# Kernel tuning notes

Measured on AMD Instinct MI355X. Metric: run time of the kernel, lower is better.

The kernel has to match this reference:

```python
import jax, jax.numpy as jnp
import numpy as np

T, B, IN_DIM = 8192, 4, 512
D_V, D_K, CHUNK = 512, 64, 128
EPS = 1e-8


def setup_inputs() -> dict:
    key = jax.random.key(0)
    ks = jax.random.split(key, 9)
    s = 0.02
    return {
        "x": jax.random.normal(ks[0], (T, B, IN_DIM), jnp.float32),
        "Wv": jax.random.normal(ks[1], (D_V, IN_DIM), jnp.float32) * s,
        "bv": jnp.zeros((D_V,), jnp.float32),
        "Wk": jax.random.normal(ks[2], (D_K, IN_DIM), jnp.float32) * s,
        "bk": jnp.zeros((D_K,), jnp.float32),
        "Wq": jax.random.normal(ks[3], (D_K, IN_DIM), jnp.float32) * s,
        "bq": jnp.zeros((D_K,), jnp.float32),
        "Wa": jax.random.normal(ks[4], (D_K, IN_DIM), jnp.float32) * s,
        "ba": jnp.zeros((D_K,), jnp.float32),
    }


def reference(x, Wv, bv, Wk, bk, Wq, bq, Wa, ba):
    # Projections: x (T, B, in_dim)
    v = x @ Wv.T + bv                      # (T, B, d)
    k = x @ Wk.T + bk                      # (T, B, n)
    q = x @ Wq.T + bq                      # (T, B, n)
    alpha = jax.nn.sigmoid(x @ Wa.T + ba)  # (T, B, n) decay gates

    Tt, Bb = x.shape[0], x.shape[1]
    C = CHUNK
    nC = Tt // C  # T assumed divisible by chunk size

    def to_chunks(a):
        return a.reshape(nC, C, Bb, a.shape[-1])

    vs, ks_, qs, als = to_chunks(v), to_chunks(k), to_chunks(q), to_chunks(alpha)
    causal = jnp.tril(jnp.ones((C, C), dtype=bool))  # (C, C)

    def body(S, inp):
        v_ch, k_ch, q_ch, a_ch = inp  # each (C, B, .)
        # Cumulative decay product within chunk (clamped as in the original)
        p = jnp.cumprod(jnp.maximum(a_ch, EPS), axis=0)      # (C, B, n)
        q_t = q_ch * p                                        # (C, B, n)
        k_t = k_ch / (p + EPS)                                # (C, B, n)
        # Intra-chunk causal attention scores
        A = jnp.einsum('tbn,sbn->bts', q_t, k_t)              # (B, C, C)
        A = jnp.where(causal[None, :, :], A, jnp.zeros((), A.dtype))
        y = jnp.einsum('bts,sbd->tbd', A, v_ch)               # intra-chunk
        y = y + jnp.einsum('bdn,tbn->tbd', S, q_t)            # cross-chunk carry
        # State update to end of chunk
        p_end = p[-1]                                         # (B, n)
        S_writes = jnp.einsum('tbd,tbn->bdn', v_ch, k_t * p_end[None, :, :])
        S_new = S * p_end[:, None, :] + S_writes              # (B, d, n)
        return S_new, y

    S0 = jnp.zeros((Bb, D_V, D_K), x.dtype)
    _, ys = jax.lax.scan(body, S0, (vs, ks_, qs, als))        # ys: (nC, C, B, d)
    return ys.reshape(Tt, Bb, D_V)
```

## Files before the change

### kernel.cpp

```cpp
#include <hip/hip_runtime.h>
#include <math.h>

#define T_DIM 8192
#define B_DIM 4
#define INDIM 512
#define DV 512
#define DK 64
#define CHUNK 128
#define NCH (T_DIM / CHUNK)
#define ROWS (T_DIM * B_DIM)
#define NPAD 768
#define KCAT 192
#define EPSF 1e-8f

typedef float float4_t __attribute__((ext_vector_type(4)));
typedef short short8_t __attribute__((ext_vector_type(8)));
typedef _Float16 half8_t __attribute__((ext_vector_type(8)));

__device__ inline unsigned short f2bf(float f) {
  unsigned int u = __float_as_uint(f);
  unsigned int r = (u + 0x7fffu + ((u >> 16) & 1u)) >> 16;
  return (unsigned short)r;
}
__device__ inline float bf2f(unsigned short h) {
  return __uint_as_float(((unsigned int)h) << 16);
}
__device__ inline unsigned short f2h(float f) {
  _Float16 h = (_Float16)f;
  unsigned short u;
  __builtin_memcpy(&u, &h, 2);
  return u;
}

__device__ inline void gload16(const void* g, void* l) {
  __builtin_amdgcn_global_load_lds(
      (const __attribute__((address_space(1))) void*)g,
      (__attribute__((address_space(3))) void*)l, 16, 0, 0);
}

__global__ __launch_bounds__(256) void cast_kernel(
    const float* __restrict__ x,
    const float* __restrict__ Wv, const float* __restrict__ Wk,
    const float* __restrict__ Wq, const float* __restrict__ Wa,
    const float* __restrict__ bv, const float* __restrict__ bk,
    const float* __restrict__ bq, const float* __restrict__ ba,
    unsigned short* __restrict__ xh, unsigned short* __restrict__ wh,
    float* __restrict__ bcat)
{
  if (blockIdx.x < 16384) {
    const size_t i4 = ((size_t)blockIdx.x * 256 + threadIdx.x) * 4;
    const float4 v = *(const float4*)&x[i4];
    ushort4 h;
    h.x = f2h(v.x); h.y = f2h(v.y); h.z = f2h(v.z); h.w = f2h(v.w);
    *(ushort4*)&xh[i4] = h;
  } else {
    const int t = (blockIdx.x - 16384) * 256 + threadIdx.x;
    const size_t i4 = (size_t)t * 4;
    const int row = (int)(i4 >> 9);
    const int col = (int)(i4 & 511);
    float4 v = {0.f, 0.f, 0.f, 0.f};
    if (row < 512)      v = *(const float4*)&Wv[(size_t)row * INDIM + col];
    else if (row < 576) v = *(const float4*)&Wk[(size_t)(row - 512) * INDIM + col];
    else if (row < 640) v = *(const float4*)&Wq[(size_t)(row - 576) * INDIM + col];
    else if (row < 704) v = *(const float4*)&Wa[(size_t)(row - 640) * INDIM + col];
    ushort4 h;
    h.x = f2h(v.x); h.y = f2h(v.y); h.z = f2h(v.z); h.w = f2h(v.w);
    *(ushort4*)&wh[i4] = h;
    if (t < NPAD) {
      float b = 0.f;
      if (t < 512)      b = bv[t];
      else if (t < 576) b = bk[t - 512];
      else if (t < 640) b = bq[t - 576];
      else if (t < 704) b = ba[t - 640];
      bcat[t] = b;
    }
  }
}

__global__ __launch_bounds__(256) void proj_mfma_kernel(
    const unsigned short* __restrict__ xh, const unsigned short* __restrict__ wh,
    const float* __restrict__ bcat,
    float* __restrict__ v_ws, float* __restrict__ k_ws,
    float* __restrict__ q_ws, float* __restrict__ a_ws)
{
  __shared__ __align__(16) _Float16 Ah[3][128 * 32];
  __shared__ __align__(16) _Float16 Bh[3][128 * 32];

  const int d     = blockIdx.x;
  const int grp   = d >> 3;
  const int ytile = (d & 7) * 32 + grp / 6;
  const int xtile = grp % 6;
  const int r0 = ytile * 128;
  const int c0 = xtile * 128;

  const int tid  = threadIdx.x;
  const int wave = tid >> 6, lane = tid & 63;
  const int wm   = (wave & 1) * 64, wn = (wave >> 1) * 64;
  const int fm   = lane & 15;
  const int fk   = (lane >> 4) * 8;

  float4_t acc[4][4];
#pragma unroll
  for (int i = 0; i < 4; ++i)
#pragma unroll
    for (int j = 0; j < 4; ++j) acc[i][j] = (float4_t)0.0f;

  const int srow = tid >> 2;
  const int scol = (tid & 3) * 8;

  const unsigned short* pA0 = xh + (size_t)(r0 + srow) * INDIM + scol;
  const unsigned short* pA1 = xh + (size_t)(r0 + 64 + srow) * INDIM + scol;
  const unsigned short* pB0 = wh + (size_t)(c0 + srow) * INDIM + scol;
  const unsigned short* pB1 = wh + (size_t)(c0 + 64 + srow) * INDIM + scol;

  auto stage = [&](int buf, int k0) {
    gload16(pA0 + k0, &Ah[buf][tid * 8]);
    gload16(pA1 + k0, &Ah[buf][(256 + tid) * 8]);
    gload16(pB0 + k0, &Bh[buf][tid * 8]);
    gload16(pB1 + k0, &Bh[buf][(256 + tid) * 8]);
  };

  auto compute = [&](int buf) {
    half8_t a[4], b[4];
#pragma unroll
    for (int i = 0; i < 4; ++i)
      a[i] = *(const half8_t*)&Ah[buf][(wm + i * 16 + fm) * 32 + fk];
#pragma unroll
    for (int j = 0; j < 4; ++j)
      b[j] = *(const half8_t*)&Bh[buf][(wn + j * 16 + fm) * 32 + fk];
    __builtin_amdgcn_s_setprio(1);
#pragma unroll
    for (int i = 0; i < 4; ++i)
#pragma unroll
      for (int j = 0; j < 4; ++j)
        acc[i][j] = __builtin_amdgcn_mfma_f32_16x16x32_f16(a[i], b[j], acc[i][j], 0, 0, 0);
    __builtin_amdgcn_s_setprio(0);
  };

  stage(0, 0);
  stage(1, 32);
  int cur = 0;
  for (int t = 0; t < 14; ++t) {
    stage((cur + 2) % 3, (t + 2) * 32);
    asm volatile("s_waitcnt vmcnt(8)" ::: "memory");
    __builtin_amdgcn_s_barrier();
    compute(cur);
    __builtin_amdgcn_s_barrier();
    cur = (cur + 1) % 3;
  }
  asm volatile("s_waitcnt vmcnt(4)" ::: "memory");
  __builtin_amdgcn_s_barrier();
  compute(cur);
  cur = (cur + 1) % 3;
  asm volatile("s_waitcnt vmcnt(0)" ::: "memory");
  __builtin_amdgcn_s_barrier();
  compute(cur);

#pragma unroll
  for (int j = 0; j < 4; ++j) {
    const int col = c0 + wn + j * 16 + fm;
    if (col >= 704) continue;
    const float bias = bcat[col];
#pragma unroll
    for (int i = 0; i < 4; ++i) {
#pragma unroll
      for (int r = 0; r < 4; ++r) {
        const int row = r0 + wm + i * 16 + (lane >> 4) * 4 + r;
        const float val = acc[i][j][r] + bias;
        if (col < 512) {
          v_ws[(size_t)row * DV + col] = val;
        } else if (col < 576) {
          k_ws[(size_t)row * DK + col - 512] = val;
        } else if (col < 640) {
          q_ws[(size_t)row * DK + col - 576] = val;
        } else {
          a_ws[(size_t)row * DK + col - 640] = 1.0f / (1.0f + expf(-val));
        }
      }
    }
  }
}

__global__ __launch_bounds__(256) void prep_kernel(
    const float* __restrict__ a_ws, float* __restrict__ k_ws,
    const float* __restrict__ q_ws,
    unsigned short* __restrict__ Acat_h, unsigned short* __restrict__ Acat_l,
    float* __restrict__ pend)
{
  __shared__ float pal[CHUNK][DK];
  const int c = blockIdx.x, b = blockIdx.y;
  const int cb = c * B_DIM + b;
  const int tid = threadIdx.x;

#pragma unroll
  for (int i = 0; i < 8; ++i) {
    const int f = (i * 256 + tid) * 4;
    const int t = f >> 6, n0 = f & 63;
    const float4 av = *(const float4*)&a_ws[(size_t)(c * CHUNK + t) * 256 + b * 64 + n0];
    *(float4*)&pal[t][n0] = av;
  }
  __syncthreads();

  if (tid < 64) {
    float p = 1.0f;
#pragma unroll 4
    for (int t = 0; t < CHUNK; ++t) {
      p *= fmaxf(pal[t][tid], EPSF);
      pal[t][tid] = p;
    }
    pend[c * 256 + b * 64 + tid] = p;
  }
  __syncthreads();

#pragma unroll
  for (int i = 0; i < 8; ++i) {
    const int f = (i * 256 + tid) * 4;
    const int t = f >> 6, n0 = f & 63;
    const float4 qv = *(const float4*)&q_ws[(size_t)(c * CHUNK + t) * 256 + b * 64 + n0];
    const size_t qa = ((size_t)cb * CHUNK + t) * KCAT + 128 + n0;
    float q0 = qv.x * pal[t][n0 + 0];
    float q1 = qv.y * pal[t][n0 + 1];
    float q2 = qv.z * pal[t][n0 + 2];
    float q3 = qv.w * pal[t][n0 + 3];
    ushort4 h, l;
    h.x = f2bf(q0); l.x = f2bf(q0 - bf2f(h.x));
    h.y = f2bf(q1); l.y = f2bf(q1 - bf2f(h.y));
    h.z = f2bf(q2); l.z = f2bf(q2 - bf2f(h.z));
    h.w = f2bf(q3); l.w = f2bf(q3 - bf2f(h.w));
    *(ushort4*)&Acat_h[qa] = h;
    *(ushort4*)&Acat_l[qa] = l;
  }

#pragma unroll
  for (int i = 0; i < 8; ++i) {
    const int f = (i * 256 + tid) * 4;
    const int t = f >> 6, n0 = f & 63;
    const size_t ka = (size_t)(c * CHUNK + t) * 256 + b * 64 + n0;
    float4 kv = *(const float4*)&k_ws[ka];
    kv.x = kv.x / (pal[t][n0 + 0] + EPSF);
    kv.y = kv.y / (pal[t][n0 + 1] + EPSF);
    kv.z = kv.z / (pal[t][n0 + 2] + EPSF);
    kv.w = kv.w / (pal[t][n0 + 3] + EPSF);
    *(float4*)&k_ws[ka] = kv;
  }
}

__global__ __launch_bounds__(256) void vt_kernel(
    const float* __restrict__ v_ws,
    unsigned short* __restrict__ Bt_h, unsigned short* __restrict__ Bt_l)
{
  __shared__ float Ts[CHUNK][65];
  const int c = blockIdx.x, b = blockIdx.y, dblk = blockIdx.z;
  const int cb = c * B_DIM + b;
  const int d0 = dblk * 64;
  const int tid = threadIdx.x;
#pragma unroll
  for (int q = 0; q < 8; ++q) {
    const int idx = (q * 256 + tid) * 4;
    const int s = idx >> 6, dd = idx & 63;
    const float4 v = *(const float4*)&v_ws[(size_t)((c * CHUNK + s) * B_DIM + b) * DV + d0 + dd];
    Ts[s][dd + 0] = v.x; Ts[s][dd + 1] = v.y;
    Ts[s][dd + 2] = v.z; Ts[s][dd + 3] = v.w;
  }
  __syncthreads();
#pragma unroll
  for (int q = 0; q < 8; ++q) {
    const int idx = (q * 256 + tid) * 4;
    const int dd = idx >> 7, s0 = idx & 127;
    float v0 = Ts[s0 + 0][dd], v1 = Ts[s0 + 1][dd];
    float v2 = Ts[s0 + 2][dd], v3 = Ts[s0 + 3][dd];
    ushort4 h, l;
    h.x = f2bf(v0); l.x = f2bf(v0 - bf2f(h.x));
    h.y = f2bf(v1); l.y = f2bf(v1 - bf2f(h.y));
    h.z = f2bf(v2); l.z = f2bf(v2 - bf2f(h.z));
    h.w = f2bf(v3); l.w = f2bf(v3 - bf2f(h.w));
    const size_t oa = ((size_t)cb * DV + d0 + dd) * CHUNK + s0;
    *(ushort4*)&Bt_h[oa] = h;
    *(ushort4*)&Bt_l[oa] = l;
  }
}

__global__ __launch_bounds__(256) void wchunk_mfma_kernel(
    const unsigned short* __restrict__ Bt_h, const unsigned short* __restrict__ Bt_l,
    const float* __restrict__ k_ws, const float* __restrict__ pend,
    float* __restrict__ W_ws)
{
  __shared__ __align__(16) unsigned short Ah[128 * 32];
  __shared__ __align__(16) unsigned short Al[128 * 32];

  const int c = blockIdx.x, b = blockIdx.y, dt = blockIdx.z;
  const int cb = c * B_DIM + b;
  const int tid  = threadIdx.x;
  const int wave = tid >> 6, lane = tid & 63;
  const int wm   = (wave & 1) * 64;
  const int wn   = (wave >> 1) * 32;
  const int fm   = lane & 15;
  const int fk   = (lane >> 4) * 8;

  const unsigned short* Ab_h = Bt_h + ((size_t)cb * DV + dt * 128) * CHUNK;
  const unsigned short* Ab_l = Bt_l + ((size_t)cb * DV + dt * 128) * CHUNK;

  float4_t acc[4][2];
#pragma unroll
  for (int i = 0; i < 4; ++i)
#pragma unroll
    for (int j = 0; j < 2; ++j) acc[i][j] = (float4_t)0.0f;

  for (int ks = 0; ks < 4; ++ks) {
    const int k0 = ks * 32;
#pragma unroll
    for (int q = 0; q < 2; ++q) {
      const int flat = (q * 256 + tid) * 8;
      const int row = flat >> 5, col = flat & 31;
      gload16(&Ab_h[(size_t)row * CHUNK + k0 + col], &Ah[flat]);
      gload16(&Ab_l[(size_t)row * CHUNK + k0 + col], &Al[flat]);
    }

    short8_t b_hi[2], b_lo[2];
#pragma unroll
    for (int j = 0; j < 2; ++j) {
      const int n = wn + j * 16 + fm;
#pragma unroll
      for (int e = 0; e < 8; ++e) {
        const float kv = k_ws[(size_t)(c * CHUNK + k0 + fk + e) * 256 + b * 64 + n];
        const unsigned short h = f2bf(kv);
        b_hi[j][e] = (short)h;
        b_lo[j][e] = (short)f2bf(kv - bf2f(h));
      }
    }
    __syncthreads();

    short8_t a_hi[4], a_lo[4];
#pragma unroll
    for (int i = 0; i < 4; ++i) {
      const int ar = (wm + i * 16 + fm) * 32 + fk;
      a_hi[i] = *(const short8_t*)&Ah[ar];
      a_lo[i] = *(const short8_t*)&Al[ar];
    }
#pragma unroll
    for (int i = 0; i < 4; ++i)
#pragma unroll
      for (int j = 0; j < 2; ++j) {
        acc[i][j] = __builtin_amdgcn_mfma_f32_16x16x32_bf16(a_hi[i], b_hi[j], acc[i][j], 0, 0, 0);
        acc[i][j] = __builtin_amdgcn_mfma_f32_16x16x32_bf16(a_lo[i], b_hi[j], acc[i][j], 0, 0, 0);
        acc[i][j] = __builtin_amdgcn_mfma_f32_16x16x32_bf16(a_hi[i], b_lo[j], acc[i][j], 0, 0, 0);
      }
    __syncthreads();
  }

#pragma unroll
  for (int j = 0; j < 2; ++j) {
    const int n = wn + j * 16 + fm;
    const float pj = pend[c * 256 + b * 64 + n];
#pragma unroll
    for (int i = 0; i < 4; ++i) {
#pragma unroll
      for (int r = 0; r < 4; ++r) {
        const int d = dt * 128 + wm + i * 16 + (lane >> 4) * 4 + r;
        W_ws[((size_t)cb * DV + d) * DK + n] = acc[i][j][r] * pj;
      }
    }
  }
}

__global__ __launch_bounds__(256) void scan_kernel(
    const float* __restrict__ W_ws, const float* __restrict__ pend,
    unsigned short* __restrict__ Sh, unsigned short* __restrict__ Sl)
{
  const int flat = blockIdx.x * 256 + threadIdx.x;
  const int n = flat & 63;
  const int bd = flat >> 6;
  const int b = bd >> 9;
  float s = 0.0f;
  for (int c = 0; c < NCH; ++c) {
    const int off = c * 131072 + flat;
    const float w = W_ws[off];
    const unsigned short h = f2bf(s);
    Sh[off] = h;
    Sl[off] = f2bf(s - bf2f(h));
    s = s * pend[c * 256 + b * 64 + n] + w;
  }
}

__global__ __launch_bounds__(256) void score_mfma_kernel(
    const float* __restrict__ k_ws,
    unsigned short* __restrict__ Acat_h, unsigned short* __restrict__ Acat_l)
{
  __shared__ __align__(16) unsigned short Ah[128 * 64];
  __shared__ __align__(16) unsigned short Al[128 * 64];
  __shared__ __align__(16) unsigned short Bh[128 * 64];
  __shared__ __align__(16) unsigned short Bl[128 * 64];

  const int c = blockIdx.x, b = blockIdx.y;
  const int cb = c * B_DIM + b;
  const int tid  = threadIdx.x;
  const int wave = tid >> 6, lane = tid & 63;
  const int wm   = (wave & 1) * 64, wn = (wave >> 1) * 64;
  const int fm   = lane & 15;
  const int fk   = (lane >> 4) * 8;

  const unsigned short* Aq_h = Acat_h + (size_t)cb * CHUNK * KCAT + 128;
  const unsigned short* Aq_l = Acat_l + (size_t)cb * CHUNK * KCAT + 128;

  const int srow = tid >> 3;
  const int scolB = (tid & 7) * 16;
  const int sc = (scolB ^ ((srow & 7) << 4)) >> 1;
  const int sdst = srow * 64 + (scolB >> 1);
#pragma unroll
  for (int q = 0; q < 4; ++q) {
    const int row = q * 32 + srow;
    const int dst = q * 2048 + sdst;
    gload16(&Aq_h[(size_t)row * KCAT + sc], &Ah[dst]);
    gload16(&Aq_l[(size_t)row * KCAT + sc], &Al[dst]);
  }
#pragma unroll
  for (int q = 0; q < 8; ++q) {
    const int f = (q * 256 + tid) * 4;
    const int s = f >> 6, n0 = f & 63;
    const float4 kv = *(const float4*)&k_ws[(size_t)(c * CHUNK + s) * 256 + b * 64 + n0];
    ushort4 h, l;
    h.x = f2bf(kv.x); l.x = f2bf(kv.x - bf2f(h.x));
    h.y = f2bf(kv.y); l.y = f2bf(kv.y - bf2f(h.y));
    h.z = f2bf(kv.z); l.z = f2bf(kv.z - bf2f(h.z));
    h.w = f2bf(kv.w); l.w = f2bf(kv.w - bf2f(h.w));
    const int wi = s * 64 + (n0 ^ ((s & 7) << 3));
    *(ushort4*)&Bh[wi] = h;
    *(ushort4*)&Bl[wi] = l;
  }
  __syncthreads();

  float4_t acc[4][4];
#pragma unroll
  for (int i = 0; i < 4; ++i)
#pragma unroll
    for (int j = 0; j < 4; ++j) acc[i][j] = (float4_t)0.0f;

#pragma unroll
  for (int ksub = 0; ksub < 2; ++ksub) {
    short8_t a_hi[4], a_lo[4], b_hi[4], b_lo[4];
#pragma unroll
    for (int i = 0; i < 4; ++i) {
      const int r = wm + i * 16 + fm;
      const int ar = r * 64 + ((ksub * 32 + fk) ^ ((r & 7) << 3));
      a_hi[i] = *(const short8_t*)&Ah[ar];
      a_lo[i] = *(const short8_t*)&Al[ar];
    }
#pragma unroll
    for (int j = 0; j < 4; ++j) {
      const int r = wn + j * 16 + fm;
      const int br = r * 64 + ((ksub * 32 + fk) ^ ((r & 7) << 3));
      b_hi[j] = *(const short8_t*)&Bh[br];
      b_lo[j] = *(const short8_t*)&Bl[br];
    }
    __builtin_amdgcn_s_setprio(1);
#pragma unroll
    for (int i = 0; i < 4; ++i)
#pragma unroll
      for (int j = 0; j < 4; ++j) {
        acc[i][j] = __builtin_amdgcn_mfma_f32_16x16x32_bf16(a_hi[i], b_hi[j], acc[i][j], 0, 0, 0);
        acc[i][j] = __builtin_amdgcn_mfma_f32_16x16x32_bf16(a_lo[i], b_hi[j], acc[i][j], 0, 0, 0);
        acc[i][j] = __builtin_amdgcn_mfma_f32_16x16x32_bf16(a_hi[i], b_lo[j], acc[i][j], 0, 0, 0);
      }
    __builtin_amdgcn_s_setprio(0);
  }

#pragma unroll
  for (int j = 0; j < 4; ++j) {
    const int s = wn + j * 16 + fm;
#pragma unroll
    for (int i = 0; i < 4; ++i) {
#pragma unroll
      for (int r = 0; r < 4; ++r) {
        const int t = wm + i * 16 + (lane >> 4) * 4 + r;
        const float vv = (s <= t) ? acc[i][j][r] : 0.0f;
        const unsigned short h = f2bf(vv);
        const size_t oa = ((size_t)cb * CHUNK + t) * KCAT + s;
        Acat_h[oa] = h;
        Acat_l[oa] = f2bf(vv - bf2f(h));
      }
    }
  }
}

__global__ __launch_bounds__(256) void out_mfma_kernel(
    const unsigned short* __restrict__ Acat_h, const unsigned short* __restrict__ Acat_l,
    const unsigned short* __restrict__ Bt_h, const unsigned short* __restrict__ Bt_l,
    const unsigned short* __restrict__ Sh, const unsigned short* __restrict__ Sl,
    float* __restrict__ out)
{
  __shared__ __align__(16) unsigned short Ah[128 * 64];
  __shared__ __align__(16) unsigned short Al[128 * 64];
  __shared__ __align__(16) unsigned short Bh[128 * 64];
  __shared__ __align__(16) unsigned short Bl[128 * 64];

  const int c = blockIdx.x, b = blockIdx.y, nt = blockIdx.z;
  const int cb = c * B_DIM + b;
  const int tid  = threadIdx.x;
  const int wave = tid >> 6, lane = tid & 63;
  const int wm   = (wave & 1) * 64, wn = (wave >> 1) * 64;
  const int fm   = lane & 15;
  const int fk   = (lane >> 4) * 8;

  const unsigned short* Ab_h = Acat_h + (size_t)cb * CHUNK * KCAT;
  const unsigned short* Ab_l = Acat_l + (size_t)cb * CHUNK * KCAT;
  const unsigned short* Bb_h = Bt_h + ((size_t)cb * DV + nt * 128) * CHUNK;
  const unsigned short* Bb_l = Bt_l + ((size_t)cb * DV + nt * 128) * CHUNK;
  const unsigned short* Sb_h = Sh + ((size_t)cb * DV + nt * 128) * DK;
  const unsigned short* Sb_l = Sl + ((size_t)cb * DV + nt * 128) * DK;

  const int srow = tid >> 3;
  const int scolB = (tid & 7) * 16;
  const int sc = (scolB ^ ((srow & 7) << 4)) >> 1;
  const int sdst = srow * 64 + (scolB >> 1);

  float4_t acc[4][4];
#pragma unroll
  for (int i = 0; i < 4; ++i)
#pragma unroll
    for (int j = 0; j < 4; ++j) acc[i][j] = (float4_t)0.0f;

  for (int ks = 0; ks < 3; ++ks) {
    const int k0 = ks * 64;
#pragma unroll
    for (int q = 0; q < 4; ++q) {
      const int row = q * 32 + srow;
      const int dst = q * 2048 + sdst;
      gload16(&Ab_h[(size_t)row * KCAT + k0 + sc], &Ah[dst]);
      gload16(&Ab_l[(size_t)row * KCAT + k0 + sc], &Al[dst]);
      if (ks < 2) {
        gload16(&Bb_h[(size_t)row * CHUNK + k0 + sc], &Bh[dst]);
        gload16(&Bb_l[(size_t)row * CHUNK + k0 + sc], &Bl[dst]);
      } else {
        gload16(&Sb_h[(size_t)row * DK + sc], &Bh[dst]);
        gload16(&Sb_l[(size_t)row * DK + sc], &Bl[dst]);
      }
    }
    __syncthreads();

#pragma unroll
    for (int ksub = 0; ksub < 2; ++ksub) {
      short8_t a_hi[4], a_lo[4], b_hi[4], b_lo[4];
#pragma unroll
      for (int i = 0; i < 4; ++i) {
        const int r = wm + i * 16 + fm;
        const int ar = r * 64 + ((ksub * 32 + fk) ^ ((r & 7) << 3));
        a_hi[i] = *(const short8_t*)&Ah[ar];
        a_lo[i] = *(const short8_t*)&Al[ar];
      }
#pragma unroll
      for (int j = 0; j < 4; ++j) {
        const int r = wn + j * 16 + fm;
        const int br = r * 64 + ((ksub * 32 + fk) ^ ((r & 7) << 3));
        b_hi[j] = *(const short8_t*)&Bh[br];
        b_lo[j] = *(const short8_t*)&Bl[br];
      }
      __builtin_amdgcn_s_setprio(1);
#pragma unroll
      for (int i = 0; i < 4; ++i)
#pragma unroll
        for (int j = 0; j < 4; ++j) {
          acc[i][j] = __builtin_amdgcn_mfma_f32_16x16x32_bf16(a_hi[i], b_hi[j], acc[i][j], 0, 0, 0);
          acc[i][j] = __builtin_amdgcn_mfma_f32_16x16x32_bf16(a_lo[i], b_hi[j], acc[i][j], 0, 0, 0);
          acc[i][j] = __builtin_amdgcn_mfma_f32_16x16x32_bf16(a_hi[i], b_lo[j], acc[i][j], 0, 0, 0);
        }
      __builtin_amdgcn_s_setprio(0);
    }
    __syncthreads();
  }

#pragma unroll
  for (int j = 0; j < 4; ++j) {
    const int d = nt * 128 + wn + j * 16 + fm;
#pragma unroll
    for (int i = 0; i < 4; ++i) {
#pragma unroll
      for (int r = 0; r < 4; ++r) {
        const int t = c * CHUNK + wm + i * 16 + (lane >> 4) * 4 + r;
        out[((size_t)t * B_DIM + b) * DV + d] = acc[i][j][r];
      }
    }
  }
}

extern "C" void kernel_launch(void* const* d_in, const int* in_sizes, int n_in,
                              void* d_out, int out_size, void* d_ws, size_t ws_size,
                              hipStream_t stream)
{
  const float* x  = (const float*)d_in[0];
  const float* Wv = (const float*)d_in[1];
  const float* bv = (const float*)d_in[2];
  const float* Wk = (const float*)d_in[3];
  const float* bk = (const float*)d_in[4];
  const float* Wq = (const float*)d_in[5];
  const float* bq = (const float*)d_in[6];
  const float* Wa = (const float*)d_in[7];
  const float* ba = (const float*)d_in[8];
  float* out = (float*)d_out;

  float* ws   = (float*)d_ws;
  float* v_ws = ws;
  float* k_ws = v_ws + (size_t)ROWS * DV;
  float* a_ws = k_ws + (size_t)ROWS * DK;
  float* pend = a_ws + (size_t)ROWS * DK;
  float* W_ws = pend + NCH * B_DIM * DK;
  float* bcat = W_ws + (size_t)NCH * B_DIM * DV * DK;
  unsigned short* Acat_h = (unsigned short*)(bcat + NPAD);
  unsigned short* Acat_l = Acat_h + (size_t)NCH * B_DIM * CHUNK * KCAT;
  unsigned short* uni = Acat_l + (size_t)NCH * B_DIM * CHUNK * KCAT;
  unsigned short* xh = uni;
  unsigned short* wh = xh + (size_t)ROWS * INDIM;
  float* q_ws = (float*)(uni + (size_t)18 * 1024 * 1024);
  unsigned short* Bt_h = uni;
  unsigned short* Bt_l = Bt_h + (size_t)NCH * B_DIM * DV * CHUNK;
  unsigned short* S_h = (unsigned short*)v_ws;
  unsigned short* S_l = S_h + (size_t)NCH * B_DIM * DV * DK;

  cast_kernel<<<16384 + 384, 256, 0, stream>>>(
      x, Wv, Wk, Wq, Wa, bv, bk, bq, ba, xh, wh, bcat);
  proj_mfma_kernel<<<(ROWS / 128) * (NPAD / 128), 256, 0, stream>>>(
      xh, wh, bcat, v_ws, k_ws, q_ws, a_ws);
  prep_kernel<<<dim3(NCH, B_DIM), 256, 0, stream>>>(
      a_ws, k_ws, q_ws, Acat_h, Acat_l, pend);
  vt_kernel<<<dim3(NCH, B_DIM, 8), 256, 0, stream>>>(v_ws, Bt_h, Bt_l);
  wchunk_mfma_kernel<<<dim3(NCH, B_DIM, 4), 256, 0, stream>>>(
      Bt_h, Bt_l, k_ws, pend, W_ws);
  scan_kernel<<<(B_DIM * DV * DK) / 256, 256, 0, stream>>>(
      W_ws, pend, S_h, S_l);
  score_mfma_kernel<<<dim3(NCH, B_DIM), 256, 0, stream>>>(
      k_ws, Acat_h, Acat_l);
  out_mfma_kernel<<<dim3(NCH, B_DIM, 4), 256, 0, stream>>>(
      Acat_h, Acat_l, Bt_h, Bt_l, S_h, S_l, out);
}
```

Measured before the change: 304.0 us.

## Fuse V transpose and bf16 split into projection epilogue, drop vt_kernel

```diff
diff --git a/kernel.cpp b/kernel.cpp
--- a/kernel.cpp
+++ b/kernel.cpp
@@ -80,8 +80,9 @@
 __global__ __launch_bounds__(256) void proj_mfma_kernel(
     const unsigned short* __restrict__ xh, const unsigned short* __restrict__ wh,
     const float* __restrict__ bcat,
-    float* __restrict__ v_ws, float* __restrict__ k_ws,
-    float* __restrict__ q_ws, float* __restrict__ a_ws)
+    unsigned short* __restrict__ Bt_h, unsigned short* __restrict__ Bt_l,
+    float* __restrict__ k_ws, float* __restrict__ q_ws,
+    float* __restrict__ a_ws)
 {
   __shared__ __align__(16) _Float16 Ah[3][128 * 32];
   __shared__ __align__(16) _Float16 Bh[3][128 * 32];
@@ -98,6 +99,7 @@
   const int wm   = (wave & 1) * 64, wn = (wave >> 1) * 64;
   const int fm   = lane & 15;
   const int fk   = (lane >> 4) * 8;
+  const int g    = lane >> 4;
 
   float4_t acc[4][4];
 #pragma unroll
@@ -156,32 +158,71 @@
   __builtin_amdgcn_s_barrier();
   compute(cur);
 
-#pragma unroll
-  for (int j = 0; j < 4; ++j) {
-    const int col = c0 + wn + j * 16 + fm;
-    if (col >= 704) continue;
-    const float bias = bcat[col];
-#pragma unroll
-    for (int i = 0; i < 4; ++i) {
-#pragma unroll
-      for (int r = 0; r < 4; ++r) {
-        const int row = r0 + wm + i * 16 + (lane >> 4) * 4 + r;
-        const float val = acc[i][j][r] + bias;
-        if (col < 512) {
-          v_ws[(size_t)row * DV + col] = val;
-        } else if (col < 576) {
-          k_ws[(size_t)row * DK + col - 512] = val;
-        } else if (col < 640) {
-          q_ws[(size_t)row * DK + col - 576] = val;
-        } else {
-          a_ws[(size_t)row * DK + col - 640] = 1.0f / (1.0f + expf(-val));
+  if (xtile < 4) {
+    unsigned int* Thl = (unsigned int*)&Ah[0][0];
+    const int t0 = r0 >> 2;
+    const int cb0 = (t0 >> 7) * 4;
+    const int s0 = t0 & 127;
+    __syncthreads();
+    for (int bb = 0; bb < 4; ++bb) {
+#pragma unroll
+      for (int j = 0; j < 4; ++j) {
+        const int d_loc = wn + j * 16 + fm;
+        const float bias = bcat[c0 + d_loc];
+#pragma unroll
+        for (int i = 0; i < 4; ++i) {
+          const int trow = (wm >> 2) + i * 4 + g;
+          const float val = acc[i][j][bb] + bias;
+          const unsigned short h = f2bf(val);
+          const unsigned short l = f2bf(val - bf2f(h));
+          Thl[d_loc * 34 + trow] = (unsigned int)h | ((unsigned int)l << 16);
         }
       }
-    }
-  }
-}
-
-__global__ __launch_bounds__(256) void prep_kernel(
+      __syncthreads();
+#pragma unroll
+      for (int q2 = 0; q2 < 4; ++q2) {
+        const int task = q2 * 256 + tid;
+        const int dd = task >> 3;
+        const int tq = task & 7;
+        const unsigned int* p = &Thl[dd * 34 + tq * 4];
+        const unsigned int w0 = p[0], w1 = p[1], w2 = p[2], w3 = p[3];
+        ushort4 hh, ll;
+        hh.x = (unsigned short)w0; ll.x = (unsigned short)(w0 >> 16);
+        hh.y = (unsigned short)w1; ll.y = (unsigned short)(w1 >> 16);
+        hh.z = (unsigned short)w2; ll.z = (unsigned short)(w2 >> 16);
+        hh.w = (unsigned short)w3; ll.w = (unsigned short)(w3 >> 16);
+        const size_t oa = ((size_t)(cb0 + bb) * DV + c0 + dd) * CHUNK + s0 + tq * 4;
+        *(ushort4*)&Bt_h[oa] = hh;
+        *(ushort4*)&Bt_l[oa] = ll;
+      }
+      __syncthreads();
+    }
+  } else {
+#pragma unroll
+    for (int j = 0; j < 4; ++j) {
+      const int col = c0 + wn + j * 16 + fm;
+      if (col >= 704) continue;
+      const float bias = bcat[col];
+#pragma unroll
+      for (int i = 0; i < 4; ++i) {
+#pragma unroll
+        for (int r = 0; r < 4; ++r) {
+          const int row = r0 + wm + i * 16 + g * 4 + r;
+          const float val = acc[i][j][r] + bias;
+          if (col < 576) {
+            k_ws[(size_t)row * DK + col - 512] = val;
+          } else if (col < 640) {
+            q_ws[(size_t)row * DK + col - 576] = val;
+          } else {
+            a_ws[(size_t)row * DK + col - 640] = 1.0f / (1.0f + expf(-val));
+          }
+        }
+      }
+    }
+  }
+}
+
+__global__ __launch_bounds__(512) void prep_kernel(
     const float* __restrict__ a_ws, float* __restrict__ k_ws,
     const float* __restrict__ q_ws,
     unsigned short* __restrict__ Acat_h, unsigned short* __restrict__ Acat_l,
@@ -193,8 +234,8 @@
   const int tid = threadIdx.x;
 
 #pragma unroll
-  for (int i = 0; i < 8; ++i) {
-    const int f = (i * 256 + tid) * 4;
+  for (int i = 0; i < 4; ++i) {
+    const int f = (i * 512 + tid) * 4;
     const int t = f >> 6, n0 = f & 63;
     const float4 av = *(const float4*)&a_ws[(size_t)(c * CHUNK + t) * 256 + b * 64 + n0];
     *(float4*)&pal[t][n0] = av;
@@ -213,8 +254,8 @@
   __syncthreads();
 
 #pragma unroll
-  for (int i = 0; i < 8; ++i) {
-    const int f = (i * 256 + tid) * 4;
+  for (int i = 0; i < 4; ++i) {
+    const int f = (i * 512 + tid) * 4;
     const int t = f >> 6, n0 = f & 63;
     const float4 qv = *(const float4*)&q_ws[(size_t)(c * CHUNK + t) * 256 + b * 64 + n0];
     const size_t qa = ((size_t)cb * CHUNK + t) * KCAT + 128 + n0;
@@ -232,8 +273,8 @@
   }
 
 #pragma unroll
-  for (int i = 0; i < 8; ++i) {
-    const int f = (i * 256 + tid) * 4;
+  for (int i = 0; i < 4; ++i) {
+    const int f = (i * 512 + tid) * 4;
     const int t = f >> 6, n0 = f & 63;
     const size_t ka = (size_t)(c * CHUNK + t) * 256 + b * 64 + n0;
     float4 kv = *(const float4*)&k_ws[ka];
@@ -245,41 +286,6 @@
   }
 }
 
-__global__ __launch_bounds__(256) void vt_kernel(
-    const float* __restrict__ v_ws,
-    unsigned short* __restrict__ Bt_h, unsigned short* __restrict__ Bt_l)
-{
-  __shared__ float Ts[CHUNK][65];
-  const int c = blockIdx.x, b = blockIdx.y, dblk = blockIdx.z;
-  const int cb = c * B_DIM + b;
-  const int d0 = dblk * 64;
-  const int tid = threadIdx.x;
-#pragma unroll
-  for (int q = 0; q < 8; ++q) {
-    const int idx = (q * 256 + tid) * 4;
-    const int s = idx >> 6, dd = idx & 63;
-    const float4 v = *(const float4*)&v_ws[(size_t)((c * CHUNK + s) * B_DIM + b) * DV + d0 + dd];
-    Ts[s][dd + 0] = v.x; Ts[s][dd + 1] = v.y;
-    Ts[s][dd + 2] = v.z; Ts[s][dd + 3] = v.w;
-  }
-  __syncthreads();
-#pragma unroll
-  for (int q = 0; q < 8; ++q) {
-    const int idx = (q * 256 + tid) * 4;
-    const int dd = idx >> 7, s0 = idx & 127;
-    float v0 = Ts[s0 + 0][dd], v1 = Ts[s0 + 1][dd];
-    float v2 = Ts[s0 + 2][dd], v3 = Ts[s0 + 3][dd];
-    ushort4 h, l;
-    h.x = f2bf(v0); l.x = f2bf(v0 - bf2f(h.x));
-    h.y = f2bf(v1); l.y = f2bf(v1 - bf2f(h.y));
-    h.z = f2bf(v2); l.z = f2bf(v2 - bf2f(h.z));
-    h.w = f2bf(v3); l.w = f2bf(v3 - bf2f(h.w));
-    const size_t oa = ((size_t)cb * DV + d0 + dd) * CHUNK + s0;
-    *(ushort4*)&Bt_h[oa] = h;
-    *(ushort4*)&Bt_l[oa] = l;
-  }
-}
-
 __global__ __launch_bounds__(256) void wchunk_mfma_kernel(
     const unsigned short* __restrict__ Bt_h, const unsigned short* __restrict__ Bt_l,
     const float* __restrict__ k_ws, const float* __restrict__ pend,
@@ -288,8 +294,10 @@
   __shared__ __align__(16) unsigned short Ah[128 * 32];
   __shared__ __align__(16) unsigned short Al[128 * 32];
 
-  const int c = blockIdx.x, b = blockIdx.y, dt = blockIdx.z;
-  const int cb = c * B_DIM + b;
+  const int bd = blockIdx.x;
+  const int cb = (bd >> 5) * 8 + (bd & 7);
+  const int dt = (bd >> 3) & 3;
+  const int c = cb >> 2, b = cb & 3;
   const int tid  = threadIdx.x;
   const int wave = tid >> 6, lane = tid & 63;
   const int wm   = (wave & 1) * 64;
@@ -356,8 +364,8 @@
     for (int i = 0; i < 4; ++i) {
 #pragma unroll
       for (int r = 0; r < 4; ++r) {
-        const int d = dt * 128 + wm + i * 16 + (lane >> 4) * 4 + r;
-        W_ws[((size_t)cb * DV + d) * DK + n] = acc[i][j][r] * pj;
+        const int dd = dt * 128 + wm + i * 16 + (lane >> 4) * 4 + r;
+        W_ws[((size_t)cb * DV + dd) * DK + n] = acc[i][j][r] * pj;
       }
     }
   }
@@ -493,8 +501,10 @@
   __shared__ __align__(16) unsigned short Bh[128 * 64];
   __shared__ __align__(16) unsigned short Bl[128 * 64];
 
-  const int c = blockIdx.x, b = blockIdx.y, nt = blockIdx.z;
-  const int cb = c * B_DIM + b;
+  const int bd = blockIdx.x;
+  const int cb = (bd >> 5) * 8 + (bd & 7);
+  const int nt = (bd >> 3) & 3;
+  const int c = cb >> 2, b = cb & 3;
   const int tid  = threadIdx.x;
   const int wave = tid >> 6, lane = tid & 63;
   const int wm   = (wave & 1) * 64, wn = (wave >> 1) * 64;
@@ -598,8 +608,9 @@
   float* out = (float*)d_out;
 
   float* ws   = (float*)d_ws;
-  float* v_ws = ws;
-  float* k_ws = v_ws + (size_t)ROWS * DV;
+  unsigned short* Bt_h = (unsigned short*)ws;
+  unsigned short* Bt_l = Bt_h + (size_t)NCH * B_DIM * DV * CHUNK;
+  float* k_ws = ws + (size_t)ROWS * DV;
   float* a_ws = k_ws + (size_t)ROWS * DK;
   float* pend = a_ws + (size_t)ROWS * DK;
   float* W_ws = pend + NCH * B_DIM * DK;
@@ -610,24 +621,21 @@
   unsigned short* xh = uni;
   unsigned short* wh = xh + (size_t)ROWS * INDIM;
   float* q_ws = (float*)(uni + (size_t)18 * 1024 * 1024);
-  unsigned short* Bt_h = uni;
-  unsigned short* Bt_l = Bt_h + (size_t)NCH * B_DIM * DV * CHUNK;
-  unsigned short* S_h = (unsigned short*)v_ws;
+  unsigned short* S_h = uni;
   unsigned short* S_l = S_h + (size_t)NCH * B_DIM * DV * DK;
 
   cast_kernel<<<16384 + 384, 256, 0, stream>>>(
       x, Wv, Wk, Wq, Wa, bv, bk, bq, ba, xh, wh, bcat);
   proj_mfma_kernel<<<(ROWS / 128) * (NPAD / 128), 256, 0, stream>>>(
-      xh, wh, bcat, v_ws, k_ws, q_ws, a_ws);
-  prep_kernel<<<dim3(NCH, B_DIM), 256, 0, stream>>>(
+      xh, wh, bcat, Bt_h, Bt_l, k_ws, q_ws, a_ws);
+  prep_kernel<<<dim3(NCH, B_DIM), 512, 0, stream>>>(
       a_ws, k_ws, q_ws, Acat_h, Acat_l, pend);
-  vt_kernel<<<dim3(NCH, B_DIM, 8), 256, 0, stream>>>(v_ws, Bt_h, Bt_l);
-  wchunk_mfma_kernel<<<dim3(NCH, B_DIM, 4), 256, 0, stream>>>(
+  wchunk_mfma_kernel<<<NCH * B_DIM * 4, 256, 0, stream>>>(
       Bt_h, Bt_l, k_ws, pend, W_ws);
   scan_kernel<<<(B_DIM * DV * DK) / 256, 256, 0, stream>>>(
       W_ws, pend, S_h, S_l);
   score_mfma_kernel<<<dim3(NCH, B_DIM), 256, 0, stream>>>(
       k_ws, Acat_h, Acat_l);
-  out_mfma_kernel<<<dim3(NCH, B_DIM, 4), 256, 0, stream>>>(
+  out_mfma_kernel<<<NCH * B_DIM * 4, 256, 0, stream>>>(
       Acat_h, Acat_l, Bt_h, Bt_l, S_h, S_l, out);
 }
```

Result: faster. 269.9 us (-11.2%).
